# Optimization experiments

Hardware: AMD Instinct MI355X
Metric: run time of the kernel (lower is better)

The kernel has to match this reference:

```python
import jax, jax.numpy as jnp
import numpy as np
import math

EPS = 1e-5
H = 8  # n_heads


def _layernorm(x, g, b):
    mu = jnp.mean(x, axis=-1, keepdims=True)
    var = jnp.var(x, axis=-1, keepdims=True)
    return (x - mu) * jax.lax.rsqrt(var + EPS) * g + b


def _conv1d(x_bdn, w_oik):
    # x: [B, D, N], w: [O, I, K] (torch Conv1d layout), padding = K//2
    k = w_oik.shape[-1]
    p = k // 2
    return jax.lax.conv_general_dilated(
        x_bdn, w_oik, window_strides=(1,), padding=((p, p),),
        dimension_numbers=('NCH', 'OIH', 'NCH'))


def setup_inputs() -> dict:
    key = jax.random.key(0)
    ks = jax.random.split(key, 10)
    B, N, D, dq = 4096, 25, 256, 64
    s = 0.02
    inp = {
        'x': jax.random.normal(ks[0], (B, N, D), jnp.float32),
        'wq': jax.random.normal(ks[1], (D, D, 3), jnp.float32) * s,
        'wk': jax.random.normal(ks[2], (D, D, 3), jnp.float32) * s,
        'wv': jax.random.normal(ks[3], (D, D, 3), jnp.float32) * s,
        'ln_q_g': jnp.ones((D,), jnp.float32), 'ln_q_b': jnp.zeros((D,), jnp.float32),
        'ln_k_g': jnp.ones((D,), jnp.float32), 'ln_k_b': jnp.zeros((D,), jnp.float32),
        'ln_v_g': jnp.ones((D,), jnp.float32), 'ln_v_b': jnp.zeros((D,), jnp.float32),
        'rel_table': jax.random.normal(ks[4], (2 * N - 1, H), jnp.float32) * s,
        'global_bias': jax.random.normal(ks[5], (H, N, N), jnp.float32) * s,
        'alpha': jnp.float32(1.0),
        'wqf': jax.random.normal(ks[6], (D, dq), jnp.float32) * s,
        'bqf': jnp.zeros((dq,), jnp.float32),
        'wqp': jax.random.normal(ks[7], (dq, H), jnp.float32) * s,
        'bqp': jnp.zeros((H,), jnp.float32),
        'wo': jax.random.normal(ks[8], (D, D), jnp.float32) * s,
        'bo': jnp.zeros((D,), jnp.float32),
    }
    return inp


def reference(x, wq, wk, wv, ln_q_g, ln_q_b, ln_k_g, ln_k_b, ln_v_g, ln_v_b,
              rel_table, global_bias, alpha, wqf, bqf, wqp, bqp, wo, bo):
    B, N, D = x.shape
    dk = D // H
    xp = jnp.transpose(x, (0, 2, 1))  # [B, D, N]

    # conv projections + LayerNorm + residual
    q = x + _layernorm(jnp.transpose(_conv1d(xp, wq), (0, 2, 1)), ln_q_g, ln_q_b)
    k = x + _layernorm(jnp.transpose(_conv1d(xp, wk), (0, 2, 1)), ln_k_g, ln_k_b)
    v = x + _layernorm(jnp.transpose(_conv1d(xp, wv), (0, 2, 1)), ln_v_g, ln_v_b)

    q4 = q.reshape(B, N, H, dk)
    k4 = k.reshape(B, N, H, dk)
    v4 = v.reshape(B, N, H, dk)

    scores = jnp.einsum('bnhd,bmhd->bhnm', q4, k4) / math.sqrt(dk)

    # relative position bias: table[(i - j) + N - 1] -> [H, N, N]
    ids = jnp.arange(N)
    rel_idx = ids[:, None] - ids[None, :] + N - 1  # [N, N]
    rel_bias = jnp.transpose(rel_table[rel_idx], (2, 0, 1))  # [H, N, N]
    scores = scores + rel_bias[None] + global_bias[None] * alpha

    # dynamic adjacency bias from pairwise node feature differences
    qf = x @ wqf + bqf  # [B, N, dq]
    pair = jnp.tanh(qf[:, :, None, :] - qf[:, None, :, :])  # [B, N, N, dq]
    dyn = pair @ wqp + bqp  # [B, N, N, H]
    scores = scores + jnp.transpose(dyn, (0, 3, 1, 2))

    attn = jax.nn.softmax(scores, axis=-1)  # [B, H, N, N]
    out = jnp.einsum('bhnm,bmhd->bnhd', attn, v4).reshape(B, N, D)
    return out @ wo + bo
```

## Files before the change

### kernel.cpp

```cpp
#include <hip/hip_runtime.h>
#include <hip/hip_bf16.h>
#include <stdint.h>

using u16 = unsigned short;
using u32 = unsigned int;

typedef __attribute__((ext_vector_type(8))) __bf16 bf16x8;
typedef __attribute__((ext_vector_type(4))) float f32x4;

__device__ __forceinline__ float bf2f(u16 h) {
  u32 u = ((u32)h) << 16;
  return __builtin_bit_cast(float, u);
}
__device__ __forceinline__ u16 f2bf(float f) {
  u32 u = __builtin_bit_cast(u32, f);
  u += 0x7fffu + ((u >> 16) & 1u);
  return (u16)(u >> 16);
}
__device__ __forceinline__ float blo(u32 u) { return __builtin_bit_cast(float, u << 16); }
__device__ __forceinline__ float bhi(u32 u) { return __builtin_bit_cast(float, u & 0xffff0000u); }

__device__ __forceinline__ uint4 cvt8(const float* s) {
  float4 f0 = *(const float4*)s;
  float4 f1 = *(const float4*)(s + 4);
  uint4 r;
  r.x = (u32)f2bf(f0.x) | ((u32)f2bf(f0.y) << 16);
  r.y = (u32)f2bf(f0.z) | ((u32)f2bf(f0.w) << 16);
  r.z = (u32)f2bf(f1.x) | ((u32)f2bf(f1.y) << 16);
  r.w = (u32)f2bf(f1.z) | ((u32)f2bf(f1.w) << 16);
  return r;
}

__device__ __forceinline__ u32 tanh2(u32 a, u32 b) {
  const float d0 = blo(a) - blo(b);
  const float d1 = bhi(a) - bhi(b);
  const float e0 = __expf(2.f * d0), e1 = __expf(2.f * d1);
  const float t0 = 1.f - 2.f * __builtin_amdgcn_rcpf(e0 + 1.f);
  const float t1 = 1.f - 2.f * __builtin_amdgcn_rcpf(e1 + 1.f);
  return (u32)f2bf(t0) | ((u32)f2bf(t1) << 16);
}

__device__ __forceinline__ void gl_lds(const u16* gsrc, u16* ldsbase) {
  __builtin_amdgcn_global_load_lds(
      (const __attribute__((address_space(1))) u32*)gsrc,
      (__attribute__((address_space(3))) u32*)ldsbase, 16, 0, 0);
}


__global__ __launch_bounds__(256) void prep_kernel(
    const float* __restrict__ wq, const float* __restrict__ wk, const float* __restrict__ wv,
    const float* __restrict__ wo, const float* __restrict__ wqf,
    const float* __restrict__ lnqg, const float* __restrict__ lnqb,
    const float* __restrict__ lnkg, const float* __restrict__ lnkb,
    const float* __restrict__ lnvg, const float* __restrict__ lnvb,
    const float* __restrict__ relt, const float* __restrict__ gbias,
    const float* __restrict__ alphap,
    const float* __restrict__ wqp, const float* __restrict__ bqp,
    const float* __restrict__ bqf, const float* __restrict__ bo,
    u16* __restrict__ wT, u16* __restrict__ woT,
    u16* __restrict__ wqfT, u16* __restrict__ params)
{
  long long j = (long long)blockIdx.x * 256 + threadIdx.x;
  if (j < 589824) {
    int col = (int)(j / 768), k = (int)(j % 768);
    int p = col >> 8, o = col & 255, t = k >> 8, i = k & 255;
    const float* w = (p == 0) ? wq : (p == 1) ? wk : wv;
    wT[j] = f2bf(w[o * 768 + i * 3 + t]);
    return;
  }
  j -= 589824;
  if (j < 65536) {
    int n = (int)(j >> 8), k = (int)(j & 255);
    woT[j] = f2bf(wo[k * 256 + n]);
    return;
  }
  j -= 65536;
  if (j < 16384) {
    int col = (int)(j >> 8), k = (int)(j & 255);
    wqfT[j] = f2bf(wqf[k * 64 + col]);
    return;
  }
  j -= 16384;
  if (j < 8864) {
    int t = (int)j;
    if (t >= 8800) { params[t] = 0; return; }
    if (t >= 7776) {
      int t2 = t - 7776;
      int col = t2 >> 6, k = t2 & 63;
      params[t] = (col < 8) ? f2bf(wqp[k * 8 + col]) : (u16)0;
      return;
    }
    if (t >= 1928 && t < 6928) {
      int idx = t - 1928;
      int h = idx / 625, rem = idx % 625, n = rem / 25, m = rem % 25;
      params[t] = f2bf(gbias[idx] * alphap[0] + relt[(n - m + 24) * 8 + h] + bqp[h]);
      return;
    }
    const float* src; int si;
    if (t < 1536) {
      int a = t >> 8, c = t & 255;
      src = (a == 0) ? lnqg : (a == 1) ? lnqb : (a == 2) ? lnkg
          : (a == 3) ? lnkb : (a == 4) ? lnvg : lnvb;
      si = c;
    } else if (t < 1928) { src = relt;  si = t - 1536; }
    else if (t < 6936)   { src = alphap; si = 0; }
    else if (t < 7448)   { src = wqp;   si = t - 6936; }
    else if (t < 7456)   { src = bqp;   si = t - 7448; }
    else if (t < 7520)   { src = bqf;   si = t - 7456; }
    else                 { src = bo;    si = t - 7520; }
    params[t] = f2bf(src[si]);
  }
}

__global__ __launch_bounds__(256) void xconv_kernel(
    const float* __restrict__ x, u16* __restrict__ xbf)
{
  const long long i = ((long long)blockIdx.x * 256 + threadIdx.x) * 8;
  *(uint4*)&xbf[i] = cvt8(x + i);
}

__global__ __launch_bounds__(256) void convln_kernel(
    const u16* __restrict__ xbf, long long row0,
    const u16* __restrict__ wT, const u16* __restrict__ wqfT,
    u16* __restrict__ C,
    u16* __restrict__ qfc,
    const u16* __restrict__ params,
    const u16* __restrict__ zpad,
    int ny)
{
  __shared__ __align__(16) u16 Asm[64 * 64];
  __shared__ __align__(16) u16 Bsm[256 * 64];
  __shared__ float sG[256];
  __shared__ float sB[256];
  __shared__ float sSum[4][64];
  __shared__ float sSq[4][64];

  const int tid = threadIdx.x;
  const int l = tid & 63, w = tid >> 6;
  const int lrow = l >> 3, chunk = l & 7;
  const int l15 = l & 15;
  const int rbase = 4 * (l >> 4);
  const int swz = l15 & 7;

  if ((int)blockIdx.x < 3 * ny) {
    const int ny8 = ny & ~7;
    int p, y;
    if ((int)blockIdx.x < 3 * ny8) {
      const int g = blockIdx.x / 24, r2 = blockIdx.x % 24;
      p = r2 >> 3;
      y = g * 8 + (r2 & 7);
    } else {
      const int b2 = blockIdx.x - 3 * ny8;
      const int nt = ny - ny8;
      p = b2 / nt;
      y = ny8 + b2 % nt;
    }
    const int c0 = p * 256;
    const int r0 = y * 64;

    sG[tid] = bf2f(params[p * 512 + tid]);
    sB[tid] = bf2f(params[p * 512 + 256 + tid]);

    f32x4 acc[4][4];
#pragma unroll
    for (int m = 0; m < 4; ++m)
#pragma unroll
      for (int n = 0; n < 4; ++n)
        acc[m][n] = (f32x4){0.f, 0.f, 0.f, 0.f};

    for (int ks = 0; ks < 12; ++ks) {
      const int k0 = ks * 64;
      const int t = k0 >> 8, kc = k0 & 255;
      __syncthreads();
#pragma unroll
      for (int it = 0; it < 2; ++it) {
        const int seg = w * 2 + it;
        const int row_l = seg * 8 + lrow;
        const bool valid = ((unsigned)((r0 + row_l) % 25 + t - 1) < 25u);
        const u16* src = valid
            ? xbf + (size_t)(row0 + r0 + row_l + t - 1) * 256 + kc + ((chunk ^ lrow) << 3)
            : zpad;
        gl_lds(src, &Asm[seg * 512]);
      }
#pragma unroll
      for (int it = 0; it < 8; ++it) {
        const int seg = w * 8 + it;
        const int row_l = seg * 8 + lrow;
        const u16* src = wT + (size_t)(c0 + row_l) * 768 + k0 + ((chunk ^ lrow) << 3);
        gl_lds(src, &Bsm[seg * 512]);
      }
      __syncthreads();

#pragma unroll
      for (int kk = 0; kk < 64; kk += 32) {
        const int c = (kk >> 3) + (l >> 4);
        const int co = ((c ^ swz) << 3);
        bf16x8 av[4], bv[4];
#pragma unroll
        for (int m = 0; m < 4; ++m)
          av[m] = *(const bf16x8*)&Asm[(m * 16 + l15) * 64 + co];
#pragma unroll
        for (int n = 0; n < 4; ++n)
          bv[n] = *(const bf16x8*)&Bsm[(w * 64 + n * 16 + l15) * 64 + co];
#pragma unroll
        for (int m = 0; m < 4; ++m)
#pragma unroll
          for (int n = 0; n < 4; ++n)
            acc[m][n] = __builtin_amdgcn_mfma_f32_16x16x32_bf16(av[m], bv[n], acc[m][n], 0, 0, 0);
      }
    }

#pragma unroll
    for (int m = 0; m < 4; ++m) {
#pragma unroll
      for (int r = 0; r < 4; ++r) {
        float s = 0.f, q = 0.f;
#pragma unroll
        for (int n = 0; n < 4; ++n) { const float v = acc[m][n][r]; s += v; q += v * v; }
#pragma unroll
        for (int mk = 1; mk < 16; mk <<= 1) {
          s += __shfl_xor(s, mk, 64);
          q += __shfl_xor(q, mk, 64);
        }
        if (l15 == 0) {
          const int row = m * 16 + rbase + r;
          sSum[w][row] = s;
          sSq[w][row] = q;
        }
      }
    }
    __syncthreads();

#pragma unroll
    for (int m = 0; m < 4; ++m) {
      float mu4[4], rs4[4];
#pragma unroll
      for (int r = 0; r < 4; ++r) {
        const int row = m * 16 + rbase + r;
        const float tot = sSum[0][row] + sSum[1][row] + sSum[2][row] + sSum[3][row];
        const float tq  = sSq[0][row] + sSq[1][row] + sSq[2][row] + sSq[3][row];
        const float mu = tot * (1.f / 256.f);
        const float var = tq * (1.f / 256.f) - mu * mu;
        mu4[r] = mu;
        rs4[r] = rsqrtf(var + 1e-5f);
      }
#pragma unroll
      for (int n = 0; n < 4; ++n) {
        const int lc = w * 64 + n * 16 + l15;
        const float g = sG[lc], bb = sB[lc];
#pragma unroll
        for (int r = 0; r < 4; ++r) {
          const int row = m * 16 + rbase + r;
          const float xv = bf2f(xbf[(size_t)(row0 + r0 + row) * 256 + lc]);
          const float v = (acc[m][n][r] - mu4[r]) * rs4[r] * g + bb + xv;
          C[(size_t)(r0 + row) * 768 + c0 + lc] = f2bf(v);
        }
      }
    }
  } else {
    const int r0 = (blockIdx.x - 3 * ny) * 64;

    f32x4 acc2[4];
#pragma unroll
    for (int n = 0; n < 4; ++n) acc2[n] = (f32x4){0.f, 0.f, 0.f, 0.f};

    for (int ki = 0; ki < 4; ++ki) {
      __syncthreads();
#pragma unroll
      for (int it = 0; it < 2; ++it) {
        const int seg = w * 2 + it;
        const int row_l = seg * 8 + lrow;
        const u16* src = xbf + (size_t)(row0 + r0 + row_l) * 256 + ki * 64
                       + ((chunk ^ lrow) << 3);
        gl_lds(src, &Asm[seg * 512]);
      }
#pragma unroll
      for (int it = 0; it < 2; ++it) {
        const int seg = w * 2 + it;
        const int row_l = seg * 8 + lrow;
        const u16* src = wqfT + (size_t)row_l * 256 + ki * 64 + ((chunk ^ lrow) << 3);
        gl_lds(src, &Bsm[seg * 512]);
      }
      __syncthreads();

#pragma unroll
      for (int kk = 0; kk < 64; kk += 32) {
        const int c = (kk >> 3) + (l >> 4);
        const int co = ((c ^ swz) << 3);
        const bf16x8 av = *(const bf16x8*)&Asm[(w * 16 + l15) * 64 + co];
#pragma unroll
        for (int n = 0; n < 4; ++n) {
          const bf16x8 bv = *(const bf16x8*)&Bsm[(n * 16 + l15) * 64 + co];
          acc2[n] = __builtin_amdgcn_mfma_f32_16x16x32_bf16(av, bv, acc2[n], 0, 0, 0);
        }
      }
    }
#pragma unroll
    for (int n = 0; n < 4; ++n) {
      const int col = n * 16 + l15;
      const float badd = bf2f(params[7456 + col]);
#pragma unroll
      for (int r = 0; r < 4; ++r) {
        const int row = r0 + w * 16 + rbase + r;
        qfc[(size_t)row * 64 + col] = f2bf(acc2[n][r] + badd);
      }
    }
  }
}

template<int BN, bool HAS_BIAS, bool F32OUT, bool XCDP>
__global__ __launch_bounds__(256) void gemm_kernel(
    const u16* __restrict__ A, int lda, long long row0,
    const u16* __restrict__ BT, int ldb,
    void* __restrict__ Cv, int ldc,
    const u16* __restrict__ bias,
    int ksteps, int ncols)
{
  constexpr int NB = BN / 32;
  __shared__ __align__(16) u16 Asm[128 * 64];
  __shared__ __align__(16) u16 Bsm[BN * 64];

  const int tid = threadIdx.x;
  const int l = tid & 63;
  const int w = tid >> 6;

  int c0, r0;
  if constexpr (XCDP) {
    const int ny = gridDim.x / ncols;
    const int ny8 = ny & ~7;
    const int grp = ncols * 8;
    int cx, y;
    if ((int)blockIdx.x < ncols * ny8) {
      const int g = blockIdx.x / grp, r2 = blockIdx.x % grp;
      cx = r2 >> 3;
      y = g * 8 + (r2 & 7);
    } else {
      const int b2 = blockIdx.x - ncols * ny8;
      const int nt = ny - ny8;
      cx = b2 / nt;
      y = ny8 + b2 % nt;
    }
    c0 = cx * BN;
    r0 = y * 128;
  } else {
    c0 = blockIdx.x * BN;
    r0 = blockIdx.y * 128;
  }
  const int wr = w >> 1, wc = w & 1;

  f32x4 acc[4][NB];
#pragma unroll
  for (int m = 0; m < 4; ++m)
#pragma unroll
    for (int n = 0; n < NB; ++n)
      acc[m][n] = (f32x4){0.f, 0.f, 0.f, 0.f};

  const int lrow = l >> 3;
  const int chunk = l & 7;
  const int l15 = l & 15;
  const int swz = l15 & 7;

  for (int ks = 0; ks < ksteps; ++ks) {
    const int k0 = ks * 64;
    __syncthreads();
#pragma unroll
    for (int it = 0; it < 4; ++it) {
      const int seg = w * 4 + it;
      const int row_l = seg * 8 + lrow;
      const u16* src = A + (size_t)(row0 + r0 + row_l) * lda + k0 + ((chunk ^ lrow) << 3);
      gl_lds(src, &Asm[seg * 512]);
    }
#pragma unroll
    for (int it = 0; it < NB; ++it) {
      const int seg = w * NB + it;
      const int row_l = seg * 8 + lrow;
      const u16* src = BT + (size_t)(c0 + row_l) * ldb + k0 + ((chunk ^ lrow) << 3);
      gl_lds(src, &Bsm[seg * 512]);
    }
    __syncthreads();

#pragma unroll
    for (int kk = 0; kk < 64; kk += 32) {
      const int c = (kk >> 3) + (l >> 4);
      const int co = ((c ^ swz) << 3);
      bf16x8 av[4], bv[NB];
#pragma unroll
      for (int m = 0; m < 4; ++m)
        av[m] = *(const bf16x8*)&Asm[(wr * 64 + m * 16 + l15) * 64 + co];
#pragma unroll
      for (int n = 0; n < NB; ++n)
        bv[n] = *(const bf16x8*)&Bsm[(wc * (BN / 2) + n * 16 + l15) * 64 + co];
#pragma unroll
      for (int m = 0; m < 4; ++m)
#pragma unroll
        for (int n = 0; n < NB; ++n)
          acc[m][n] = __builtin_amdgcn_mfma_f32_16x16x32_bf16(av[m], bv[n], acc[m][n], 0, 0, 0);
    }
  }

  const int rbase = 4 * (l >> 4);
#pragma unroll
  for (int m = 0; m < 4; ++m) {
#pragma unroll
    for (int n = 0; n < NB; ++n) {
      const int col = c0 + wc * (BN / 2) + n * 16 + l15;
      float badd = 0.f;
      if (HAS_BIAS) badd = bf2f(bias[col]);
#pragma unroll
      for (int r = 0; r < 4; ++r) {
        const int row = r0 + wr * 64 + m * 16 + rbase + r;
        const float v = acc[m][n][r] + badd;
        if constexpr (F32OUT) ((float*)Cv)[(size_t)row * ldc + col] = v;
        else                  ((u16*)Cv)[(size_t)row * ldc + col] = f2bf(v);
      }
    }
  }
}

__global__ __launch_bounds__(256) void attn_kernel(
    u16* __restrict__ qkv,
    const u16* __restrict__ qf,
    const u16* __restrict__ params)
{
  __shared__ __align__(16) char arena[38848];
  float* sS    = (float*)arena;
  u16*   sV    = (u16*)(arena + 20000);
  u16*   sQF   = (u16*)(arena + 33200);
  u16*   sWQPT = (u16*)(arena + 36800);

  const int b = blockIdx.x;
  const int tid = threadIdx.x;
  const int w = tid >> 6, l = tid & 63;
  const int g8 = (l >> 4) * 8;
  const int rbase = 4 * (l >> 4);
  const int l15 = l & 15;

  {
    for (int i = tid; i < 800; i += 256) {
      const int m = i >> 5, c8 = (i & 31) * 8;
      *(uint4*)&sV[m * 264 + c8] =
          *(const uint4*)(qkv + (size_t)(b * 25 + m) * 768 + 512 + c8);
    }
    for (int i = tid; i < 200; i += 256) {
      const int r = i >> 3, c8 = (i & 7) * 8;
      *(uint4*)&sQF[r * 72 + c8] = *(const uint4*)(qf + (size_t)b * 1600 + r * 64 + c8);
    }
    for (int i = tid; i < 128; i += 256)
      ((uint4*)sWQPT)[i] = ((const uint4*)(params + 7776))[i];
  }
  __syncthreads();

  f32x4 dt[10];
  {
    const bf16x8 bv0 = *(const bf16x8*)&sWQPT[l15 * 64 + g8];
    const bf16x8 bv1 = *(const bf16x8*)&sWQPT[l15 * 64 + 32 + g8];
#pragma unroll
    for (int ti = 0; ti < 10; ++ti) {
      const int p0 = (ti * 4 + w) * 16;
      int p = p0 + l15; if (p > 624) p = 624;
      const int n = p / 25, m = p % 25;
      const uint4 qn0 = *(const uint4*)&sQF[n * 72 + g8];
      const uint4 qn1 = *(const uint4*)&sQF[n * 72 + 32 + g8];
      const uint4 qm0 = *(const uint4*)&sQF[m * 72 + g8];
      const uint4 qm1 = *(const uint4*)&sQF[m * 72 + 32 + g8];
      u32 a0[4], a1[4];
      a0[0] = tanh2(qn0.x, qm0.x); a0[1] = tanh2(qn0.y, qm0.y);
      a0[2] = tanh2(qn0.z, qm0.z); a0[3] = tanh2(qn0.w, qm0.w);
      a1[0] = tanh2(qn1.x, qm1.x); a1[1] = tanh2(qn1.y, qm1.y);
      a1[2] = tanh2(qn1.z, qm1.z); a1[3] = tanh2(qn1.w, qm1.w);
      const bf16x8 av0 = __builtin_bit_cast(bf16x8, *(uint4*)a0);
      const bf16x8 av1 = __builtin_bit_cast(bf16x8, *(uint4*)a1);
      f32x4 d = (f32x4){0.f, 0.f, 0.f, 0.f};
      d = __builtin_amdgcn_mfma_f32_16x16x32_bf16(av0, bv0, d, 0, 0, 0);
      d = __builtin_amdgcn_mfma_f32_16x16x32_bf16(av1, bv1, d, 0, 0, 0);
      dt[ti] = d;
    }
    bf16x8 zf8;
#pragma unroll
    for (int j = 0; j < 8; ++j) zf8[j] = (__bf16)0.f;
#pragma unroll
    for (int hh = 0; hh < 2; ++hh) {
      const int h = 2 * w + hh;
      bf16x8 qa[2], kb[2];
#pragma unroll
      for (int t = 0; t < 2; ++t) {
        const int row = l15 + 16 * t;
        if (row < 25) {
          const u16* base = qkv + (size_t)(b * 25 + row) * 768 + h * 32 + g8;
          qa[t] = *(const bf16x8*)base;
          kb[t] = *(const bf16x8*)(base + 256);
        } else { qa[t] = zf8; kb[t] = zf8; }
      }
#pragma unroll
      for (int tn = 0; tn < 2; ++tn)
#pragma unroll
        for (int tm = 0; tm < 2; ++tm) {
          f32x4 d = __builtin_amdgcn_mfma_f32_16x16x32_bf16(
              qa[tn], kb[tm], (f32x4){0.f, 0.f, 0.f, 0.f}, 0, 0, 0);
          const int m = l15 + 16 * tm;
#pragma unroll
          for (int r = 0; r < 4; ++r) {
            const int n = rbase + r + 16 * tn;
            if (n < 25 && m < 25) {
              const int idx = h * 625 + n * 25 + m;
              sS[idx] = d[r] * 0.17677669529663687f + bf2f(params[1928 + idx]);
            }
          }
        }
    }
  }
  __syncthreads();

  {
    if (l15 < 8) {
      const int h = l15;
#pragma unroll
      for (int ti = 0; ti < 10; ++ti) {
        const int p0 = (ti * 4 + w) * 16;
#pragma unroll
        for (int r = 0; r < 4; ++r) {
          const int p = p0 + rbase + r;
          if (p < 625) sS[h * 625 + p] += dt[ti][r];
        }
      }
    }
  }
  __syncthreads();

  {
    for (int u = tid; u < 200; u += 256) {
      const int h = u / 25, n = u % 25;
      float* rp = &sS[h * 625 + n * 25];
      float mx = -1e30f;
#pragma unroll
      for (int m = 0; m < 25; ++m) mx = fmaxf(mx, rp[m]);
      float ssum = 0.f;
#pragma unroll
      for (int m = 0; m < 25; ++m) { rp[m] = __expf(rp[m] - mx); ssum += rp[m]; }
      const float inv = __builtin_amdgcn_rcpf(ssum);
#pragma unroll
      for (int m = 0; m < 25; ++m) rp[m] *= inv;
    }
  }
  __syncthreads();

  {
#pragma unroll
    for (int hh = 0; hh < 2; ++hh) {
      const int h = 2 * w + hh;
      bf16x8 pa[2], vb[2];
#pragma unroll
      for (int t = 0; t < 2; ++t) {
        const int n = l15 + 16 * t;
#pragma unroll
        for (int j = 0; j < 8; ++j) {
          const int m = g8 + j;
          const float pv = (n < 25 && m < 25) ? sS[h * 625 + n * 25 + m] : 0.f;
          pa[t][j] = (__bf16)pv;
        }
      }
#pragma unroll
      for (int t = 0; t < 2; ++t) {
        const int dcol = l15 + 16 * t;
#pragma unroll
        for (int j = 0; j < 8; ++j) {
          const int m = g8 + j;
          vb[t][j] = (m < 25)
              ? __builtin_bit_cast(__bf16, sV[m * 264 + h * 32 + dcol])
              : (__bf16)0.f;
        }
      }
#pragma unroll
      for (int tn = 0; tn < 2; ++tn)
#pragma unroll
        for (int td = 0; td < 2; ++td) {
          f32x4 d = __builtin_amdgcn_mfma_f32_16x16x32_bf16(
              pa[tn], vb[td], (f32x4){0.f, 0.f, 0.f, 0.f}, 0, 0, 0);
          const int dcol = l15 + 16 * td;
#pragma unroll
          for (int r = 0; r < 4; ++r) {
            const int n = rbase + r + 16 * tn;
            if (n < 25)
              qkv[(size_t)(b * 25 + n) * 768 + h * 32 + dcol] = f2bf(d[r]);
          }
        }
    }
  }
}

extern "C" void kernel_launch(void* const* d_in, const int* in_sizes, int n_in,
                              void* d_out, int out_size, void* d_ws, size_t ws_size,
                              hipStream_t stream) {
  (void)in_sizes; (void)n_in; (void)out_size;
  const float* x    = (const float*)d_in[0];
  const float* wq   = (const float*)d_in[1];
  const float* wk   = (const float*)d_in[2];
  const float* wv   = (const float*)d_in[3];
  const float* lnqg = (const float*)d_in[4];
  const float* lnqb = (const float*)d_in[5];
  const float* lnkg = (const float*)d_in[6];
  const float* lnkb = (const float*)d_in[7];
  const float* lnvg = (const float*)d_in[8];
  const float* lnvb = (const float*)d_in[9];
  const float* relt = (const float*)d_in[10];
  const float* gbias= (const float*)d_in[11];
  const float* alph = (const float*)d_in[12];
  const float* wqf  = (const float*)d_in[13];
  const float* bqf  = (const float*)d_in[14];
  const float* wqp  = (const float*)d_in[15];
  const float* bqp  = (const float*)d_in[16];
  const float* wo   = (const float*)d_in[17];
  const float* bo   = (const float*)d_in[18];

  char* ws = (char*)d_ws;
  u16* params = (u16*)(ws + 0);
  u16* wT     = (u16*)(ws + 32768);
  u16* woT    = (u16*)(ws + 1212416);
  u16* wqfT   = (u16*)(ws + 1343488);
  const size_t fixed_bytes = 1376256;
  const size_t xbf_bytes = 52428800;
  const size_t per_batch = 41600;
  u16* zpad = params + 8800;

  int CB = 4096;
  while (CB > 128 && fixed_bytes + xbf_bytes + (size_t)CB * per_batch > ws_size) CB >>= 1;
  const int nchunks = 4096 / CB;
  const int rows = CB * 25;

  u16* x_bf = (u16*)(ws + fixed_bytes);
  const size_t chunk_off = fixed_bytes + xbf_bytes;
  u16* qkv_c = (u16*)(ws + chunk_off);
  u16* qf_c  = (u16*)(ws + chunk_off + (size_t)CB * 38400);
  float* outf = (float*)d_out;

  prep_kernel<<<2659, 256, 0, stream>>>(
      wq, wk, wv, wo, wqf, lnqg, lnqb, lnkg, lnkb, lnvg, lnvb,
      relt, gbias, alph, wqp, bqp, bqf, bo,
      wT, woT, wqfT, params);
  xconv_kernel<<<12800, 256, 0, stream>>>(x, x_bf);

  for (int c = 0; c < nchunks; ++c) {
    const long long R0 = (long long)c * rows;
    const int ny = rows / 64;

    convln_kernel<<<4 * ny, 256, 0, stream>>>(
        x_bf, R0, wT, wqfT, qkv_c, qf_c, params, zpad, ny);

    attn_kernel<<<CB, 256, 0, stream>>>(qkv_c, qf_c, params);

    gemm_kernel<128, true, true, true><<<2 * (rows / 128), 256, 0, stream>>>(
        qkv_c, 768, 0, woT, 256, outf + (size_t)R0 * 256, 256, params + 7520, 4, 2);
  }
}
```

Measured before the change: 361.5 us.

## Fuse output projection into attention kernel, drop separate GEMM launch

Fuses the final output projection (attn_out @ wo + bo) into the attention kernel. Each block stages its 25x256 attention result in shared memory as bf16, then runs MFMA against woT and writes fp32 output directly. This removes the qkv write-back, the re-read, and one GEMM launch per chunk. In exchange, woT is read straight from global memory with no LDS tiling and only 25 useful rows out of a 32-row MFMA tile, so reuse is lower than in the standalone GEMM.

```diff
diff --git a/kernel.cpp b/kernel.cpp
--- a/kernel.cpp
+++ b/kernel.cpp
@@ -308,119 +308,12 @@
   }
 }
 
-template<int BN, bool HAS_BIAS, bool F32OUT, bool XCDP>
-__global__ __launch_bounds__(256) void gemm_kernel(
-    const u16* __restrict__ A, int lda, long long row0,
-    const u16* __restrict__ BT, int ldb,
-    void* __restrict__ Cv, int ldc,
-    const u16* __restrict__ bias,
-    int ksteps, int ncols)
-{
-  constexpr int NB = BN / 32;
-  __shared__ __align__(16) u16 Asm[128 * 64];
-  __shared__ __align__(16) u16 Bsm[BN * 64];
-
-  const int tid = threadIdx.x;
-  const int l = tid & 63;
-  const int w = tid >> 6;
-
-  int c0, r0;
-  if constexpr (XCDP) {
-    const int ny = gridDim.x / ncols;
-    const int ny8 = ny & ~7;
-    const int grp = ncols * 8;
-    int cx, y;
-    if ((int)blockIdx.x < ncols * ny8) {
-      const int g = blockIdx.x / grp, r2 = blockIdx.x % grp;
-      cx = r2 >> 3;
-      y = g * 8 + (r2 & 7);
-    } else {
-      const int b2 = blockIdx.x - ncols * ny8;
-      const int nt = ny - ny8;
-      cx = b2 / nt;
-      y = ny8 + b2 % nt;
-    }
-    c0 = cx * BN;
-    r0 = y * 128;
-  } else {
-    c0 = blockIdx.x * BN;
-    r0 = blockIdx.y * 128;
-  }
-  const int wr = w >> 1, wc = w & 1;
-
-  f32x4 acc[4][NB];
-#pragma unroll
-  for (int m = 0; m < 4; ++m)
-#pragma unroll
-    for (int n = 0; n < NB; ++n)
-      acc[m][n] = (f32x4){0.f, 0.f, 0.f, 0.f};
-
-  const int lrow = l >> 3;
-  const int chunk = l & 7;
-  const int l15 = l & 15;
-  const int swz = l15 & 7;
-
-  for (int ks = 0; ks < ksteps; ++ks) {
-    const int k0 = ks * 64;
-    __syncthreads();
-#pragma unroll
-    for (int it = 0; it < 4; ++it) {
-      const int seg = w * 4 + it;
-      const int row_l = seg * 8 + lrow;
-      const u16* src = A + (size_t)(row0 + r0 + row_l) * lda + k0 + ((chunk ^ lrow) << 3);
-      gl_lds(src, &Asm[seg * 512]);
-    }
-#pragma unroll
-    for (int it = 0; it < NB; ++it) {
-      const int seg = w * NB + it;
-      const int row_l = seg * 8 + lrow;
-      const u16* src = BT + (size_t)(c0 + row_l) * ldb + k0 + ((chunk ^ lrow) << 3);
-      gl_lds(src, &Bsm[seg * 512]);
-    }
-    __syncthreads();
-
-#pragma unroll
-    for (int kk = 0; kk < 64; kk += 32) {
-      const int c = (kk >> 3) + (l >> 4);
-      const int co = ((c ^ swz) << 3);
-      bf16x8 av[4], bv[NB];
-#pragma unroll
-      for (int m = 0; m < 4; ++m)
-        av[m] = *(const bf16x8*)&Asm[(wr * 64 + m * 16 + l15) * 64 + co];
-#pragma unroll
-      for (int n = 0; n < NB; ++n)
-        bv[n] = *(const bf16x8*)&Bsm[(wc * (BN / 2) + n * 16 + l15) * 64 + co];
-#pragma unroll
-      for (int m = 0; m < 4; ++m)
-#pragma unroll
-        for (int n = 0; n < NB; ++n)
-          acc[m][n] = __builtin_amdgcn_mfma_f32_16x16x32_bf16(av[m], bv[n], acc[m][n], 0, 0, 0);
-    }
-  }
-
-  const int rbase = 4 * (l >> 4);
-#pragma unroll
-  for (int m = 0; m < 4; ++m) {
-#pragma unroll
-    for (int n = 0; n < NB; ++n) {
-      const int col = c0 + wc * (BN / 2) + n * 16 + l15;
-      float badd = 0.f;
-      if (HAS_BIAS) badd = bf2f(bias[col]);
-#pragma unroll
-      for (int r = 0; r < 4; ++r) {
-        const int row = r0 + wr * 64 + m * 16 + rbase + r;
-        const float v = acc[m][n][r] + badd;
-        if constexpr (F32OUT) ((float*)Cv)[(size_t)row * ldc + col] = v;
-        else                  ((u16*)Cv)[(size_t)row * ldc + col] = f2bf(v);
-      }
-    }
-  }
-}
-
 __global__ __launch_bounds__(256) void attn_kernel(
-    u16* __restrict__ qkv,
+    const u16* __restrict__ qkv,
     const u16* __restrict__ qf,
-    const u16* __restrict__ params)
+    const u16* __restrict__ params,
+    const u16* __restrict__ woT,
+    float* __restrict__ outp)
 {
   __shared__ __align__(16) char arena[38848];
   float* sS    = (float*)arena;
@@ -544,6 +437,7 @@
   }
   __syncthreads();
 
+  f32x4 od[2][2][2];
   {
 #pragma unroll
     for (int hh = 0; hh < 2; ++hh) {
@@ -573,18 +467,69 @@
 #pragma unroll
       for (int tn = 0; tn < 2; ++tn)
 #pragma unroll
+        for (int td = 0; td < 2; ++td)
+          od[hh][tn][td] = __builtin_amdgcn_mfma_f32_16x16x32_bf16(
+              pa[tn], vb[td], (f32x4){0.f, 0.f, 0.f, 0.f}, 0, 0, 0);
+    }
+  }
+  __syncthreads();
+
+  u16* sO = (u16*)arena;
+  {
+#pragma unroll
+    for (int hh = 0; hh < 2; ++hh) {
+      const int h = 2 * w + hh;
+#pragma unroll
+      for (int tn = 0; tn < 2; ++tn)
+#pragma unroll
         for (int td = 0; td < 2; ++td) {
-          f32x4 d = __builtin_amdgcn_mfma_f32_16x16x32_bf16(
-              pa[tn], vb[td], (f32x4){0.f, 0.f, 0.f, 0.f}, 0, 0, 0);
-          const int dcol = l15 + 16 * td;
+          const int dcol = h * 32 + l15 + 16 * td;
 #pragma unroll
           for (int r = 0; r < 4; ++r) {
             const int n = rbase + r + 16 * tn;
-            if (n < 25)
-              qkv[(size_t)(b * 25 + n) * 768 + h * 32 + dcol] = f2bf(d[r]);
+            if (n < 25) sO[n * 264 + dcol] = f2bf(od[hh][tn][td][r]);
           }
         }
     }
+  }
+  __syncthreads();
+
+  {
+    const int c0w = w * 64;
+    f32x4 accO[2][4];
+#pragma unroll
+    for (int t = 0; t < 2; ++t)
+#pragma unroll
+      for (int n = 0; n < 4; ++n)
+        accO[t][n] = (f32x4){0.f, 0.f, 0.f, 0.f};
+
+    for (int ks = 0; ks < 8; ++ks) {
+      bf16x8 av[2];
+#pragma unroll
+      for (int t = 0; t < 2; ++t)
+        av[t] = *(const bf16x8*)&sO[(t * 16 + l15) * 264 + ks * 32 + g8];
+#pragma unroll
+      for (int n = 0; n < 4; ++n) {
+        const bf16x8 bv = *(const bf16x8*)(woT + (size_t)(c0w + n * 16 + l15) * 256
+                                           + ks * 32 + g8);
+#pragma unroll
+        for (int t = 0; t < 2; ++t)
+          accO[t][n] = __builtin_amdgcn_mfma_f32_16x16x32_bf16(av[t], bv, accO[t][n], 0, 0, 0);
+      }
+    }
+#pragma unroll
+    for (int t = 0; t < 2; ++t)
+#pragma unroll
+      for (int n = 0; n < 4; ++n) {
+        const int col = c0w + n * 16 + l15;
+        const float badd = bf2f(params[7520 + col]);
+#pragma unroll
+        for (int r = 0; r < 4; ++r) {
+          const int row = rbase + r + 16 * t;
+          if (row < 25)
+            outp[(size_t)(b * 25 + row) * 256 + col] = accO[t][n][r] + badd;
+        }
+      }
   }
 }
 
@@ -646,9 +591,7 @@
     convln_kernel<<<4 * ny, 256, 0, stream>>>(
         x_bf, R0, wT, wqfT, qkv_c, qf_c, params, zpad, ny);
 
-    attn_kernel<<<CB, 256, 0, stream>>>(qkv_c, qf_c, params);
-
-    gemm_kernel<128, true, true, true><<<2 * (rows / 128), 256, 0, stream>>>(
-        qkv_c, 768, 0, woT, 256, outf + (size_t)R0 * 256, 256, params + 7520, 4, 2);
-  }
-}
+    attn_kernel<<<CB, 256, 0, stream>>>(
+        qkv_c, qf_c, params, woT, outf + (size_t)R0 * 256);
+  }
+}
```

Result: no change. 363.2 us (+0.5%).
